# Performance work log

Measured on AMD Instinct MI355X. Metric: run time of the kernel, lower is better.

## Reference

```python
import jax, jax.numpy as jnp
import numpy as np

B, F_DIM, H, W = 4, 256, 32, 32
DIM, DEPTH, HEADS, MLP_DIM = 768, 8, 12, 3072
DIM_HEAD = DIM // HEADS
SCALE = DIM_HEAD ** -0.5
LN_EPS = 1e-5


def sine_pos_embed(h, w, num_pos_feats):
    # PositionEmbeddingSine with normalize=True, scale=2*pi, temperature=10000
    scale = 2.0 * np.pi
    eps = 1e-6
    y = jnp.arange(1, h + 1, dtype=jnp.float32) / (h + eps) * scale  # [h]
    x = jnp.arange(1, w + 1, dtype=jnp.float32) / (w + eps) * scale  # [w]
    i = jnp.arange(num_pos_feats, dtype=jnp.float32)
    dim_t = 10000.0 ** (2.0 * jnp.floor(i / 2.0) / num_pos_feats)  # [F]

    def interleave(p):  # p: [..., F] -> sin of even dims, cos of odd dims, interleaved
        return jnp.stack([jnp.sin(p[..., 0::2]), jnp.cos(p[..., 1::2])], axis=-1).reshape(p.shape[:-1] + (-1,))

    pos_y = interleave(y[:, None] / dim_t)  # [h, F]
    pos_x = interleave(x[:, None] / dim_t)  # [w, F]
    pos = jnp.concatenate([
        jnp.broadcast_to(pos_y[:, None, :], (h, w, num_pos_feats)),
        jnp.broadcast_to(pos_x[None, :, :], (h, w, num_pos_feats)),
    ], axis=-1)  # [h, w, 2F]
    return pos.reshape(h * w, 2 * num_pos_feats)


def layer_norm(x, w, b):
    mu = jnp.mean(x, axis=-1, keepdims=True)
    var = jnp.var(x, axis=-1, keepdims=True)
    return (x - mu) * jax.lax.rsqrt(var + LN_EPS) * w + b


def setup_inputs() -> dict:
    key = jax.random.key(0)
    ks = jax.random.split(key, 16)
    s = lambda fan_in: 1.0 / np.sqrt(fan_in)
    return {
        "c_f": jax.random.normal(ks[0], (B, F_DIM, H, W), dtype=jnp.float32),
        "conv_w": jax.random.normal(ks[1], (DIM, F_DIM), dtype=jnp.float32) * s(F_DIM),
        "conv_b": jnp.zeros((DIM,), dtype=jnp.float32),
        "ln1_w": jnp.ones((DEPTH, DIM), dtype=jnp.float32),
        "ln1_b": jnp.zeros((DEPTH, DIM), dtype=jnp.float32),
        "qkv_w": jax.random.normal(ks[2], (DEPTH, DIM, 3 * DIM), dtype=jnp.float32) * s(DIM),
        "out_w": jax.random.normal(ks[3], (DEPTH, DIM, DIM), dtype=jnp.float32) * s(DIM),
        "out_b": jnp.zeros((DEPTH, DIM), dtype=jnp.float32),
        "ln2_w": jnp.ones((DEPTH, DIM), dtype=jnp.float32),
        "ln2_b": jnp.zeros((DEPTH, DIM), dtype=jnp.float32),
        "mlp_w1": jax.random.normal(ks[4], (DEPTH, DIM, MLP_DIM), dtype=jnp.float32) * s(DIM),
        "mlp_b1": jnp.zeros((DEPTH, MLP_DIM), dtype=jnp.float32),
        "mlp_w2": jax.random.normal(ks[5], (DEPTH, MLP_DIM, DIM), dtype=jnp.float32) * s(MLP_DIM),
        "mlp_b2": jnp.zeros((DEPTH, DIM), dtype=jnp.float32),
    }


def reference(c_f, conv_w, conv_b, ln1_w, ln1_b, qkv_w, out_w, out_b,
              ln2_w, ln2_b, mlp_w1, mlp_b1, mlp_w2, mlp_b2):
    b, _, h, w = c_f.shape
    n = h * w
    # 1x1 conv == per-pixel linear; tokens: [b, n, dim]
    x = jnp.einsum('bfn,df->bnd', c_f.reshape(b, F_DIM, n), conv_w) + conv_b
    x = x + sine_pos_embed(h, w, DIM // 2)[None]  # [b, n, dim]

    for l in range(DEPTH):
        # PreNorm multi-head self-attention + residual
        y = layer_norm(x, ln1_w[l], ln1_b[l])
        qkv = y @ qkv_w[l]  # [b, n, 3*dim]
        q, k, v = jnp.split(qkv, 3, axis=-1)
        to_heads = lambda t: t.reshape(b, n, HEADS, DIM_HEAD).transpose(0, 2, 1, 3)
        q, k, v = to_heads(q), to_heads(k), to_heads(v)
        dots = jnp.einsum('bhnd,bhmd->bhnm', q, k) * SCALE
        attn = jax.nn.softmax(dots, axis=-1)
        o = jnp.einsum('bhnm,bhmd->bhnd', attn, v)
        o = o.transpose(0, 2, 1, 3).reshape(b, n, DIM)
        x = o @ out_w[l] + out_b[l] + x
        # PreNorm MLP + residual
        y = layer_norm(x, ln2_w[l], ln2_b[l])
        hdd = jax.nn.gelu(y @ mlp_w1[l] + mlp_b1[l], approximate=False)
        x = hdd @ mlp_w2[l] + mlp_b2[l] + x

    return x.transpose(0, 2, 1).reshape(b, DIM, h, w)
```

## Files before the change

kernel.cpp:

```cpp
#include <hip/hip_runtime.h>
#include <stdint.h>

typedef unsigned short u16;
typedef __attribute__((ext_vector_type(8))) short short8;
typedef __attribute__((ext_vector_type(4))) short s16x4;
typedef __attribute__((ext_vector_type(4))) float f32x4;

struct P4 { float* p[4]; };

#define DEV __device__ __forceinline__

DEV u16 f2bf(float f) {
  union { float f; uint32_t u; } c; c.f = f;
  uint32_t u = c.u;
  uint32_t r = u + 0x7fffu + ((u >> 16) & 1u);
  return (u16)(r >> 16);
}

DEV void g2l16(const void* g, void* l) {
  __builtin_amdgcn_global_load_lds((__attribute__((address_space(1))) void*)(g),
                                   (__attribute__((address_space(3))) void*)(l),
                                   16, 0, 0);
}

__global__ void pos_kernel(float* __restrict__ pos) {
  int n = blockIdx.x;
  float yv = (float)((n >> 5) + 1) / (32.0f + 1e-6f) * 6.283185307179586f;
  float xv = (float)((n & 31) + 1) / (32.0f + 1e-6f) * 6.283185307179586f;
#pragma unroll
  for (int i = 0; i < 3; i++) {
    int d = threadIdx.x + i * 256;
    int dd = (d < 384) ? d : d - 384;
    float base = (d < 384) ? yv : xv;
    float ex = (float)(dd & ~1) / 384.0f;
    float arg = base / powf(10000.0f, ex);
    pos[(size_t)n * 768 + d] = (dd & 1) ? cosf(arg) : sinf(arg);
  }
}

__global__ void convw_kernel(const float* __restrict__ src, u16* __restrict__ dst) {
  int i = blockIdx.x * 256 + threadIdx.x;
  dst[i] = f2bf(src[i]);
}

DEV void tile_tr32(const float* __restrict__ src, u16* __restrict__ dst,
                   int R, int C, int tr, int tc, float (*tile)[33]) {
  int tx = threadIdx.x & 31, ty = threadIdx.x >> 5;
#pragma unroll
  for (int i = 0; i < 32; i += 8)
    tile[ty + i][tx] = src[(size_t)(tr * 32 + ty + i) * C + tc * 32 + tx];
  __syncthreads();
#pragma unroll
  for (int i = 0; i < 32; i += 8)
    dst[(size_t)(tc * 32 + ty + i) * R + tr * 32 + tx] = f2bf(tile[tx][ty + i]);
}

__global__ void wconv_kernel(const float* __restrict__ qkv_w, const float* __restrict__ out_w,
                             const float* __restrict__ m1w, const float* __restrict__ m2w,
                             u16* __restrict__ wqkv, u16* __restrict__ wout,
                             u16* __restrict__ wm1, u16* __restrict__ wm2, int layer) {
  __shared__ float tile[32][33];
  int tid = blockIdx.x;
  if (tid < 1728) {
    tile_tr32(qkv_w + (size_t)layer * 768 * 2304, wqkv, 768, 2304, tid / 72, tid % 72, tile);
  } else if (tid < 2304) {
    int t2 = tid - 1728;
    tile_tr32(out_w + (size_t)layer * 768 * 768, wout, 768, 768, t2 / 24, t2 % 24, tile);
  } else if (tid < 4608) {
    int t3 = tid - 2304;
    tile_tr32(m1w + (size_t)layer * 768 * 3072, wm1, 768, 3072, t3 / 96, t3 % 96, tile);
  } else {
    int t4 = tid - 4608;
    tile_tr32(m2w + (size_t)layer * 3072 * 768, wm2, 3072, 768, t4 / 24, t4 % 24, tile);
  }
}

__global__ void cf_tr_kernel(const float* __restrict__ c_f, u16* __restrict__ aconv) {
  __shared__ float tile[32][33];
  int b = blockIdx.z;
  tile_tr32(c_f + (size_t)b * 256 * 1024, aconv + (size_t)b * 1024 * 256,
            256, 1024, blockIdx.y, blockIdx.x, tile);
}

__global__ void out_tr_kernel(const float* __restrict__ x, float* __restrict__ out) {
  __shared__ float tile[32][33];
  int b = blockIdx.z;
  const float* src = x + (size_t)b * 1024 * 768;
  float* dst = out + (size_t)b * 768 * 1024;
  int tr = blockIdx.y, tc = blockIdx.x;
  int tx = threadIdx.x & 31, ty = threadIdx.x >> 5;
#pragma unroll
  for (int i = 0; i < 32; i += 8)
    tile[ty + i][tx] = src[(size_t)(tr * 32 + ty + i) * 768 + tc * 32 + tx];
  __syncthreads();
#pragma unroll
  for (int i = 0; i < 32; i += 8)
    dst[(size_t)(tc * 32 + ty + i) * 1024 + tr * 32 + tx] = tile[tx][ty + i];
}

__global__ __launch_bounds__(256) void ln_kernel(const float* __restrict__ x,
                                                 const float* __restrict__ w,
                                                 const float* __restrict__ bsh,
                                                 u16* __restrict__ y) {
  int row = blockIdx.x, t = threadIdx.x;
  const float* xr = x + (size_t)row * 768;
  float v[3], s = 0.f, sq = 0.f;
#pragma unroll
  for (int i = 0; i < 3; i++) { v[i] = xr[t + i * 256]; s += v[i]; sq += v[i] * v[i]; }
#pragma unroll
  for (int off = 32; off; off >>= 1) { s += __shfl_xor(s, off); sq += __shfl_xor(sq, off); }
  __shared__ float ss[4], ssq[4];
  if ((t & 63) == 0) { ss[t >> 6] = s; ssq[t >> 6] = sq; }
  __syncthreads();
  s = ss[0] + ss[1] + ss[2] + ss[3];
  sq = ssq[0] + ssq[1] + ssq[2] + ssq[3];
  float mean = s * (1.0f / 768.0f);
  float var = sq * (1.0f / 768.0f) - mean * mean;
  float rs = rsqrtf(var + 1e-5f);
#pragma unroll
  for (int i = 0; i < 3; i++) {
    int c = t + i * 256;
    y[(size_t)row * 768 + c] = f2bf((v[i] - mean) * rs * w[c] + bsh[c]);
  }
}

template <int S, bool DO_LN>
__global__ __launch_bounds__(256) void redln_kernel(P4 parts, const float* __restrict__ xin,
                                                    const float* __restrict__ bias,
                                                    const float* __restrict__ w,
                                                    const float* __restrict__ bsh,
                                                    float* __restrict__ xout,
                                                    u16* __restrict__ y) {
  int row = blockIdx.x, t = threadIdx.x;
  size_t base = (size_t)row * 768;
  float v[3], s = 0.f, sq = 0.f;
#pragma unroll
  for (int i = 0; i < 3; i++) {
    int c = t + i * 256;
    float acc = xin[base + c] + bias[c];
#pragma unroll
    for (int j = 0; j < S; j++) acc += parts.p[j][base + c];
    v[i] = acc;
    xout[base + c] = acc;
    s += acc; sq += acc * acc;
  }
  if constexpr (DO_LN) {
#pragma unroll
    for (int off = 32; off; off >>= 1) { s += __shfl_xor(s, off); sq += __shfl_xor(sq, off); }
    __shared__ float ss[4], ssq[4];
    if ((t & 63) == 0) { ss[t >> 6] = s; ssq[t >> 6] = sq; }
    __syncthreads();
    s = ss[0] + ss[1] + ss[2] + ss[3];
    sq = ssq[0] + ssq[1] + ssq[2] + ssq[3];
    float mean = s * (1.0f / 768.0f);
    float var = sq * (1.0f / 768.0f) - mean * mean;
    float rs = rsqrtf(var + 1e-5f);
#pragma unroll
    for (int i = 0; i < 3; i++) {
      int c = t + i * 256;
      y[base + c] = f2bf((v[i] - mean) * rs * w[c] + bsh[c]);
    }
  }
}

constexpr int EPI_BF16 = 0, EPI_BIAS_RES = 1, EPI_BIAS_GELU = 2, EPI_BIAS_POS = 3, EPI_PART = 4;

template <int EPI>
__global__ __launch_bounds__(256, 2) void gemm_bt(
    const u16* __restrict__ A, const u16* __restrict__ BT,
    const float* __restrict__ bias, const float* __restrict__ res,
    void* __restrict__ Cout, int M, int N, int K, P4 parts) {
  __shared__ __align__(16) u16 As[128 * 32];
  __shared__ __align__(16) u16 Bs[128 * 32];
  const int t = threadIdx.x;
  const int w = t >> 6, l = t & 63, lr = l & 15, quad = l >> 4;
  const int bm = blockIdx.y * 128, bn = blockIdx.x * 128;
  const int wm = (w & 1) * 64, wn = (w >> 1) * 64;
  f32x4 acc[4][4];
#pragma unroll
  for (int i = 0; i < 4; i++)
#pragma unroll
    for (int j = 0; j < 4; j++) acc[i][j] = (f32x4){0.f, 0.f, 0.f, 0.f};
  const int c0 = t, c1 = 256 + t;
  const size_t a0 = (size_t)(bm + (c0 >> 2)) * K + (c0 & 3) * 8;
  const size_t a1 = (size_t)(bm + (c1 >> 2)) * K + (c1 & 3) * 8;
  const size_t b0 = (size_t)(bn + (c0 >> 2)) * K + (c0 & 3) * 8;
  const size_t b1 = (size_t)(bn + (c1 >> 2)) * K + (c1 & 3) * 8;
  const int kc = K / (int)gridDim.z;
  const int kBeg = (int)blockIdx.z * kc;
  for (int k0 = kBeg; k0 < kBeg + kc; k0 += 32) {
    g2l16(A + a0 + k0, As + c0 * 8);
    g2l16(A + a1 + k0, As + c1 * 8);
    g2l16(BT + b0 + k0, Bs + c0 * 8);
    g2l16(BT + b1 + k0, Bs + c1 * 8);
    __syncthreads();
    short8 af[4], bf[4];
#pragma unroll
    for (int mi = 0; mi < 4; mi++) af[mi] = *(const short8*)(As + (wm + mi * 16 + lr) * 32 + quad * 8);
#pragma unroll
    for (int nj = 0; nj < 4; nj++) bf[nj] = *(const short8*)(Bs + (wn + nj * 16 + lr) * 32 + quad * 8);
#pragma unroll
    for (int mi = 0; mi < 4; mi++)
#pragma unroll
      for (int nj = 0; nj < 4; nj++)
        acc[mi][nj] = __builtin_amdgcn_mfma_f32_16x16x32_bf16(af[mi], bf[nj], acc[mi][nj], 0, 0, 0);
    __syncthreads();
  }
  float* Pc = (EPI == EPI_PART) ? parts.p[blockIdx.z] : nullptr;
#pragma unroll
  for (int mi = 0; mi < 4; mi++) {
    const int rowb = bm + wm + mi * 16 + quad * 4;
#pragma unroll
    for (int nj = 0; nj < 4; nj++) {
      const int gn = bn + wn + nj * 16 + lr;
#pragma unroll
      for (int r = 0; r < 4; r++) {
        const size_t idx = (size_t)(rowb + r) * N + gn;
        float v = acc[mi][nj][r];
        if constexpr (EPI == EPI_BF16) {
          ((u16*)Cout)[idx] = f2bf(v);
        } else if constexpr (EPI == EPI_BIAS_RES) {
          ((float*)Cout)[idx] = v + bias[gn] + res[idx];
        } else if constexpr (EPI == EPI_BIAS_GELU) {
          float xg = v + bias[gn];
          ((u16*)Cout)[idx] = f2bf(0.5f * xg * (1.0f + erff(xg * 0.70710678118f)));
        } else if constexpr (EPI == EPI_BIAS_POS) {
          ((float*)Cout)[idx] = v + bias[gn] + res[(size_t)((rowb + r) & 1023) * N + gn];
        } else {
          Pc[idx] = v;
        }
      }
    }
  }
}

__global__ __launch_bounds__(256) void vtr_kernel(const u16* __restrict__ qkvb,
                                                  u16* __restrict__ vT) {
  __shared__ uint32_t tile[64][65];
  const int t = threadIdx.x;
  const int bh = blockIdx.y, b = bh / 12, h = bh % 12;
  const int tok0 = blockIdx.x * 64;
  {
    int trow = t >> 2, dc = (t & 3) * 16;
    const u16* src = qkvb + (size_t)(b * 1024 + tok0 + trow) * 2304 + 1536 + h * 64 + dc;
    short8 v0 = *(const short8*)src;
    short8 v1 = *(const short8*)(src + 8);
#pragma unroll
    for (int j = 0; j < 8; j++) {
      tile[trow][dc + j] = (uint32_t)(u16)v0[j];
      tile[trow][dc + 8 + j] = (uint32_t)(u16)v1[j];
    }
  }
  __syncthreads();
  {
    int d = t >> 2, tc = (t & 3) * 16;
    short8 o0, o1;
#pragma unroll
    for (int j = 0; j < 8; j++) {
      o0[j] = (short)(u16)tile[tc + j][d];
      o1[j] = (short)(u16)tile[tc + 8 + j][d];
    }
    u16* dst = vT + (size_t)(bh * 64 + d) * 1024 + tok0 + tc;
    *(short8*)dst = o0;
    *(short8*)(dst + 8) = o1;
  }
}

__global__ __launch_bounds__(128, 3) void attn_kernel(const u16* __restrict__ qkv,
                                                      const u16* __restrict__ vT,
                                                      u16* __restrict__ o) {
  __shared__ __align__(16) u16 Ks[2 * 64 * 32];
  __shared__ __align__(16) u16 Vs[2 * 64 * 32];
  __shared__ __align__(16) u16 Ps[2][32 * 72];
  const int t = threadIdx.x;
  const int w = t >> 6, l = t & 63, lr = l & 15, quad = l >> 4;
  const int bh = blockIdx.y, b = bh / 12, h = bh % 12;
  const int qb = blockIdx.x * 64 + w * 32;

  short8 aq[2][2];
#pragma unroll
  for (int qt = 0; qt < 2; qt++)
#pragma unroll
    for (int ks = 0; ks < 2; ks++)
      aq[qt][ks] = *(const short8*)(qkv + (size_t)(b * 1024 + qb + qt * 16 + lr) * 2304 +
                                    h * 64 + ks * 32 + quad * 8);

  const u16* kbase = qkv + (size_t)(b * 1024) * 2304 + 768 + h * 64;
  const u16* vbase = vT + (size_t)(bh * 64) * 1024;
  u16* Pw = Ps[w];

  f32x4 accO[4][2];
  float l_loc[2] = {0.f, 0.f};
#pragma unroll
  for (int dj = 0; dj < 4; dj++)
#pragma unroll
    for (int qt = 0; qt < 2; qt++) accO[dj][qt] = (f32x4){0.f, 0.f, 0.f, 0.f};

  for (int kb = 0; kb < 1024; kb += 64) {
#pragma unroll
    for (int pass = 0; pass < 4; pass++) {
      int u = pass * 128 + t;
      int ks = u >> 8, row = (u >> 2) & 63, c4 = u & 3;
      g2l16(kbase + (size_t)(kb + row) * 2304 + ks * 32 + c4 * 8, Ks + (size_t)u * 8);
      g2l16(vbase + (size_t)row * 1024 + kb + ks * 32 + c4 * 8, Vs + (size_t)u * 8);
    }
    __syncthreads();

    f32x4 s[4][2];
#pragma unroll
    for (int nj = 0; nj < 4; nj++)
#pragma unroll
      for (int qt = 0; qt < 2; qt++) s[nj][qt] = (f32x4){0.f, 0.f, 0.f, 0.f};
#pragma unroll
    for (int ks = 0; ks < 2; ks++)
#pragma unroll
      for (int nj = 0; nj < 4; nj++) {
        short8 ak = *(const short8*)(Ks + ks * 2048 + (nj * 16 + lr) * 32 + quad * 8);
#pragma unroll
        for (int qt = 0; qt < 2; qt++)
          s[nj][qt] = __builtin_amdgcn_mfma_f32_16x16x32_bf16(ak, aq[qt][ks], s[nj][qt], 0, 0, 0);
      }

#pragma unroll
    for (int qt = 0; qt < 2; qt++) {
      const int rowoff = (qt * 16 + lr) * 72;
#pragma unroll
      for (int nj = 0; nj < 4; nj++) {
        s16x4 pk;
#pragma unroll
        for (int r = 0; r < 4; r++) {
          float p = exp2f(s[nj][qt][r] * 0.18033688011112042f);
          l_loc[qt] += p;
          pk[r] = (short)f2bf(p);
        }
        *(s16x4*)(Pw + rowoff + nj * 16 + quad * 4) = pk;
      }
    }

#pragma unroll
    for (int ks = 0; ks < 2; ks++) {
      short8 bp[2];
#pragma unroll
      for (int qt = 0; qt < 2; qt++)
        bp[qt] = *(const short8*)(Pw + (qt * 16 + lr) * 72 + ks * 32 + quad * 8);
#pragma unroll
      for (int dj = 0; dj < 4; dj++) {
        short8 av = *(const short8*)(Vs + ks * 2048 + (dj * 16 + lr) * 32 + quad * 8);
#pragma unroll
        for (int qt = 0; qt < 2; qt++)
          accO[dj][qt] = __builtin_amdgcn_mfma_f32_16x16x32_bf16(av, bp[qt], accO[dj][qt], 0, 0, 0);
      }
    }
    __syncthreads();
  }

#pragma unroll
  for (int qt = 0; qt < 2; qt++) {
    l_loc[qt] += __shfl_xor(l_loc[qt], 16);
    l_loc[qt] += __shfl_xor(l_loc[qt], 32);
  }
#pragma unroll
  for (int qt = 0; qt < 2; qt++) {
    float inv = 1.0f / l_loc[qt];
    size_t grow = (size_t)(b * 1024 + qb + qt * 16 + lr);
#pragma unroll
    for (int dj = 0; dj < 4; dj++) {
      s16x4 ov;
#pragma unroll
      for (int r = 0; r < 4; r++) ov[r] = (short)f2bf(accO[dj][qt][r] * inv);
      *(s16x4*)(o + grow * 768 + h * 64 + dj * 16 + quad * 4) = ov;
    }
  }
}

extern "C" void kernel_launch(void* const* d_in, const int* in_sizes, int n_in,
                              void* d_out, int out_size, void* d_ws, size_t ws_size,
                              hipStream_t stream) {
  (void)in_sizes; (void)n_in; (void)out_size;
  const float* c_f    = (const float*)d_in[0];
  const float* conv_w = (const float*)d_in[1];
  const float* conv_b = (const float*)d_in[2];
  const float* ln1_w  = (const float*)d_in[3];
  const float* ln1_b  = (const float*)d_in[4];
  const float* qkv_w  = (const float*)d_in[5];
  const float* out_w  = (const float*)d_in[6];
  const float* out_b  = (const float*)d_in[7];
  const float* ln2_w  = (const float*)d_in[8];
  const float* ln2_b  = (const float*)d_in[9];
  const float* m1w    = (const float*)d_in[10];
  const float* m1b    = (const float*)d_in[11];
  const float* m2w    = (const float*)d_in[12];
  const float* m2b    = (const float*)d_in[13];
  float* out = (float*)d_out;

  char* p = (char*)d_ws;
  auto alloc = [&](size_t bytes) { char* q = p; p += (bytes + 255) & ~(size_t)255; return q; };
  float* pos  = (float*)alloc(1024ull * 768 * 4);
  float* x    = (float*)alloc(4096ull * 768 * 4);
  u16* y      = (u16*)alloc(4096ull * 768 * 2);
  u16* qkvb   = (u16*)alloc(4096ull * 2304 * 2);
  u16* ob     = (u16*)alloc(4096ull * 768 * 2);
  u16* hb     = (u16*)alloc(4096ull * 3072 * 2);
  u16* aconv  = (u16*)alloc(4096ull * 256 * 2);
  u16* convw  = (u16*)alloc(768ull * 256 * 2);
  u16* wqkv   = (u16*)alloc(2304ull * 768 * 2);
  u16* wout   = (u16*)alloc(768ull * 768 * 2);
  u16* wm1    = (u16*)alloc(3072ull * 768 * 2);
  u16* wm2    = (u16*)alloc(768ull * 3072 * 2);
  u16* vT = hb;

  const size_t PSZ = 4096ull * 768 * 4;
  P4 parts{};
  parts.p[0] = (float*)qkvb;
  parts.p[1] = (float*)((char*)qkvb + PSZ);
  int SPLIT = 2;
  if ((size_t)(p - (char*)d_ws) + PSZ <= ws_size) {
    parts.p[2] = (float*)out;
    parts.p[3] = (float*)alloc(PSZ);
    SPLIT = 4;
  }
  P4 none{};

  pos_kernel<<<1024, 256, 0, stream>>>(pos);
  convw_kernel<<<768, 256, 0, stream>>>(conv_w, convw);
  cf_tr_kernel<<<dim3(32, 8, 4), 256, 0, stream>>>(c_f, aconv);
  gemm_bt<EPI_BIAS_POS><<<dim3(6, 32), 256, 0, stream>>>(aconv, convw, conv_b, pos, x, 4096, 768, 256, none);

  for (int lyr = 0; lyr < 8; lyr++) {
    wconv_kernel<<<6912, 256, 0, stream>>>(qkv_w, out_w, m1w, m2w, wqkv, wout, wm1, wm2, lyr);
    if (lyr == 0) {
      ln_kernel<<<4096, 256, 0, stream>>>(x, ln1_w, ln1_b, y);
    } else if (SPLIT == 4) {
      redln_kernel<4, true><<<4096, 256, 0, stream>>>(parts, x, m2b + (lyr - 1) * 768,
                                                      ln1_w + lyr * 768, ln1_b + lyr * 768, x, y);
    } else {
      redln_kernel<2, true><<<4096, 256, 0, stream>>>(parts, x, m2b + (lyr - 1) * 768,
                                                      ln1_w + lyr * 768, ln1_b + lyr * 768, x, y);
    }
    gemm_bt<EPI_BF16><<<dim3(18, 32), 256, 0, stream>>>(y, wqkv, nullptr, nullptr, qkvb, 4096, 2304, 768, none);
    vtr_kernel<<<dim3(16, 48), 256, 0, stream>>>(qkvb, vT);
    attn_kernel<<<dim3(16, 48), 128, 0, stream>>>(qkvb, vT, ob);
    gemm_bt<EPI_BIAS_RES><<<dim3(6, 32), 256, 0, stream>>>(ob, wout, out_b + lyr * 768, x, x, 4096, 768, 768, none);
    ln_kernel<<<4096, 256, 0, stream>>>(x, ln2_w + lyr * 768, ln2_b + lyr * 768, y);
    gemm_bt<EPI_BIAS_GELU><<<dim3(24, 32), 256, 0, stream>>>(y, wm1, m1b + lyr * 3072, nullptr, hb, 4096, 3072, 768, none);
    gemm_bt<EPI_PART><<<dim3(6, 32, SPLIT), 256, 0, stream>>>(hb, wm2, nullptr, nullptr, nullptr, 4096, 768, 3072, parts);
  }
  if (SPLIT == 4) {
    redln_kernel<4, false><<<4096, 256, 0, stream>>>(parts, x, m2b + 7 * 768, nullptr, nullptr, x, nullptr);
  } else {
    redln_kernel<2, false><<<4096, 256, 0, stream>>>(parts, x, m2b + 7 * 768, nullptr, nullptr, x, nullptr);
  }
  out_tr_kernel<<<dim3(24, 32, 4), 256, 0, stream>>>(x, out);
}
```

Measured before the change: 1.803 ms.

## Double-buffer K/V tiles, swizzle LDS, and use four waves per attention block

The attention kernel now runs four waves of 16 query rows each instead of two waves of 32. K/V tiles are double-buffered so the next tile's global-to-LDS load is issued before computing on the current one. The LDS column chunk is XOR-swizzled by row to reduce bank conflicts. This doubles LDS use for K/V and halves per-wave MFMA reuse of each K/V fragment, which could lower occupancy in exchange for better latency hiding. Correctness depends on the async loads finishing by the single barrier at the end of each iteration, since there is no explicit wait on the outstanding loads.

Result: faster. 1.709 ms (-5.2%).

```diff
diff --git a/kernel.cpp b/kernel.cpp
--- a/kernel.cpp
+++ b/kernel.cpp
@@ -266,71 +266,70 @@
   }
 }
 
-__global__ __launch_bounds__(128, 3) void attn_kernel(const u16* __restrict__ qkv,
+__global__ __launch_bounds__(256, 3) void attn_kernel(const u16* __restrict__ qkv,
                                                       const u16* __restrict__ vT,
                                                       u16* __restrict__ o) {
-  __shared__ __align__(16) u16 Ks[2 * 64 * 32];
-  __shared__ __align__(16) u16 Vs[2 * 64 * 32];
-  __shared__ __align__(16) u16 Ps[2][32 * 72];
+  __shared__ __align__(16) u16 Ks[2][2 * 64 * 32];
+  __shared__ __align__(16) u16 Vs[2][2 * 64 * 32];
+  __shared__ __align__(16) u16 Ps[4][16 * 72];
   const int t = threadIdx.x;
   const int w = t >> 6, l = t & 63, lr = l & 15, quad = l >> 4;
   const int bh = blockIdx.y, b = bh / 12, h = bh % 12;
-  const int qb = blockIdx.x * 64 + w * 32;
-
-  short8 aq[2][2];
-#pragma unroll
-  for (int qt = 0; qt < 2; qt++)
-#pragma unroll
-    for (int ks = 0; ks < 2; ks++)
-      aq[qt][ks] = *(const short8*)(qkv + (size_t)(b * 1024 + qb + qt * 16 + lr) * 2304 +
-                                    h * 64 + ks * 32 + quad * 8);
+  const int qb = blockIdx.x * 64 + w * 16;
+  const int swz = (lr >> 1) & 3;
+
+  short8 aq[2];
+#pragma unroll
+  for (int ks = 0; ks < 2; ks++)
+    aq[ks] = *(const short8*)(qkv + (size_t)(b * 1024 + qb + lr) * 2304 +
+                              h * 64 + ks * 32 + quad * 8);
 
   const u16* kbase = qkv + (size_t)(b * 1024) * 2304 + 768 + h * 64;
   const u16* vbase = vT + (size_t)(bh * 64) * 1024;
   u16* Pw = Ps[w];
 
-  f32x4 accO[4][2];
-  float l_loc[2] = {0.f, 0.f};
-#pragma unroll
-  for (int dj = 0; dj < 4; dj++)
-#pragma unroll
-    for (int qt = 0; qt < 2; qt++) accO[dj][qt] = (f32x4){0.f, 0.f, 0.f, 0.f};
-
+  f32x4 accO[4];
+  float l_loc = 0.f;
+#pragma unroll
+  for (int dj = 0; dj < 4; dj++) accO[dj] = (f32x4){0.f, 0.f, 0.f, 0.f};
+
+  auto stage = [&](int buf, int kb) {
+#pragma unroll
+    for (int pass = 0; pass < 2; pass++) {
+      int u = pass * 256 + t;
+      int ks = u >> 8, row = (u >> 2) & 63, c4 = u & 3;
+      int cs = c4 ^ ((row >> 1) & 3);
+      g2l16(kbase + (size_t)(kb + row) * 2304 + ks * 32 + cs * 8, Ks[buf] + (size_t)u * 8);
+      g2l16(vbase + (size_t)row * 1024 + kb + ks * 32 + cs * 8, Vs[buf] + (size_t)u * 8);
+    }
+  };
+
+  stage(0, 0);
+  __syncthreads();
+  int cur = 0;
   for (int kb = 0; kb < 1024; kb += 64) {
-#pragma unroll
-    for (int pass = 0; pass < 4; pass++) {
-      int u = pass * 128 + t;
-      int ks = u >> 8, row = (u >> 2) & 63, c4 = u & 3;
-      g2l16(kbase + (size_t)(kb + row) * 2304 + ks * 32 + c4 * 8, Ks + (size_t)u * 8);
-      g2l16(vbase + (size_t)row * 1024 + kb + ks * 32 + c4 * 8, Vs + (size_t)u * 8);
-    }
-    __syncthreads();
-
-    f32x4 s[4][2];
-#pragma unroll
-    for (int nj = 0; nj < 4; nj++)
-#pragma unroll
-      for (int qt = 0; qt < 2; qt++) s[nj][qt] = (f32x4){0.f, 0.f, 0.f, 0.f};
+    if (kb + 64 < 1024) stage(cur ^ 1, kb + 64);
+
+    f32x4 s[4];
+#pragma unroll
+    for (int nj = 0; nj < 4; nj++) s[nj] = (f32x4){0.f, 0.f, 0.f, 0.f};
 #pragma unroll
     for (int ks = 0; ks < 2; ks++)
 #pragma unroll
       for (int nj = 0; nj < 4; nj++) {
-        short8 ak = *(const short8*)(Ks + ks * 2048 + (nj * 16 + lr) * 32 + quad * 8);
-#pragma unroll
-        for (int qt = 0; qt < 2; qt++)
-          s[nj][qt] = __builtin_amdgcn_mfma_f32_16x16x32_bf16(ak, aq[qt][ks], s[nj][qt], 0, 0, 0);
+        short8 ak = *(const short8*)(Ks[cur] + ks * 2048 + (nj * 16 + lr) * 32 + (quad ^ swz) * 8);
+        s[nj] = __builtin_amdgcn_mfma_f32_16x16x32_bf16(ak, aq[ks], s[nj], 0, 0, 0);
       }
 
-#pragma unroll
-    for (int qt = 0; qt < 2; qt++) {
-      const int rowoff = (qt * 16 + lr) * 72;
+    {
+      const int rowoff = lr * 72;
 #pragma unroll
       for (int nj = 0; nj < 4; nj++) {
         s16x4 pk;
 #pragma unroll
         for (int r = 0; r < 4; r++) {
-          float p = exp2f(s[nj][qt][r] * 0.18033688011112042f);
-          l_loc[qt] += p;
+          float p = exp2f(s[nj][r] * 0.18033688011112042f);
+          l_loc += p;
           pk[r] = (short)f2bf(p);
         }
         *(s16x4*)(Pw + rowoff + nj * 16 + quad * 4) = pk;
@@ -339,35 +338,27 @@
 
 #pragma unroll
     for (int ks = 0; ks < 2; ks++) {
-      short8 bp[2];
-#pragma unroll
-      for (int qt = 0; qt < 2; qt++)
-        bp[qt] = *(const short8*)(Pw + (qt * 16 + lr) * 72 + ks * 32 + quad * 8);
+      short8 bp = *(const short8*)(Pw + lr * 72 + ks * 32 + quad * 8);
 #pragma unroll
       for (int dj = 0; dj < 4; dj++) {
-        short8 av = *(const short8*)(Vs + ks * 2048 + (dj * 16 + lr) * 32 + quad * 8);
-#pragma unroll
-        for (int qt = 0; qt < 2; qt++)
-          accO[dj][qt] = __builtin_amdgcn_mfma_f32_16x16x32_bf16(av, bp[qt], accO[dj][qt], 0, 0, 0);
+        short8 av = *(const short8*)(Vs[cur] + ks * 2048 + (dj * 16 + lr) * 32 + (quad ^ swz) * 8);
+        accO[dj] = __builtin_amdgcn_mfma_f32_16x16x32_bf16(av, bp, accO[dj], 0, 0, 0);
       }
     }
     __syncthreads();
-  }
-
-#pragma unroll
-  for (int qt = 0; qt < 2; qt++) {
-    l_loc[qt] += __shfl_xor(l_loc[qt], 16);
-    l_loc[qt] += __shfl_xor(l_loc[qt], 32);
-  }
-#pragma unroll
-  for (int qt = 0; qt < 2; qt++) {
-    float inv = 1.0f / l_loc[qt];
-    size_t grow = (size_t)(b * 1024 + qb + qt * 16 + lr);
+    cur ^= 1;
+  }
+
+  l_loc += __shfl_xor(l_loc, 16);
+  l_loc += __shfl_xor(l_loc, 32);
+  {
+    float inv = 1.0f / l_loc;
+    size_t grow = (size_t)(b * 1024 + qb + lr);
 #pragma unroll
     for (int dj = 0; dj < 4; dj++) {
       s16x4 ov;
 #pragma unroll
-      for (int r = 0; r < 4; r++) ov[r] = (short)f2bf(accO[dj][qt][r] * inv);
+      for (int r = 0; r < 4; r++) ov[r] = (short)f2bf(accO[dj][r] * inv);
       *(s16x4*)(o + grow * 768 + h * 64 + dj * 16 + quad * 4) = ov;
     }
   }
@@ -439,7 +430,7 @@
     }
     gemm_bt<EPI_BF16><<<dim3(18, 32), 256, 0, stream>>>(y, wqkv, nullptr, nullptr, qkvb, 4096, 2304, 768, none);
     vtr_kernel<<<dim3(16, 48), 256, 0, stream>>>(qkvb, vT);
-    attn_kernel<<<dim3(16, 48), 128, 0, stream>>>(qkvb, vT, ob);
+    attn_kernel<<<dim3(16, 48), 256, 0, stream>>>(qkvb, vT, ob);
     gemm_bt<EPI_BIAS_RES><<<dim3(6, 32), 256, 0, stream>>>(ob, wout, out_b + lyr * 768, x, x, 4096, 768, 768, none);
     ln_kernel<<<4096, 256, 0, stream>>>(x, ln2_w + lyr * 768, ln2_b + lyr * 768, y);
     gemm_bt<EPI_BIAS_GELU><<<dim3(24, 32), 256, 0, stream>>>(y, wm1, m1b + lyr * 3072, nullptr, hb, 4096, 3072, 768, none);
```
